# Kernel tuning notes

Measured on AMD Instinct MI355X. Metric: run time of the kernel, lower is better.

## Reference

```python
import jax, jax.numpy as jnp
import numpy as np

B, C_IN, C_OUT, N = 8, 256, 128, 4096
BN_EPS = 1e-5


def _conv1x1(w, b, t):
    # w: [out, in], t: [B, in, N] -> [B, out, N]
    return jnp.einsum('oc,bcn->bon', w, t) + b[None, :, None]


def setup_inputs() -> dict:
    key = jax.random.key(0)
    ks = jax.random.split(key, 11)
    s_in = 1.0 / np.sqrt(C_IN)
    s_out = 1.0 / np.sqrt(C_OUT)
    return {
        'x': jax.random.normal(ks[0], (B, C_IN, N), dtype=jnp.float32),
        'g_w': jax.random.normal(ks[1], (C_OUT, C_IN), dtype=jnp.float32) * s_in,
        'g_b': jax.random.normal(ks[2], (C_OUT,), dtype=jnp.float32) * s_in,
        'theta_w': jax.random.normal(ks[3], (C_OUT, C_IN), dtype=jnp.float32) * s_in,
        'theta_b': jax.random.normal(ks[4], (C_OUT,), dtype=jnp.float32) * s_in,
        'phi_w': jax.random.normal(ks[5], (C_OUT, C_IN), dtype=jnp.float32) * s_in,
        'phi_b': jax.random.normal(ks[6], (C_OUT,), dtype=jnp.float32) * s_in,
        'W_w': jax.random.normal(ks[7], (C_IN, C_OUT), dtype=jnp.float32) * s_out,
        'W_b': jax.random.normal(ks[8], (C_IN,), dtype=jnp.float32) * s_out,
        'bn_gamma': jax.random.uniform(ks[9], (C_IN,), dtype=jnp.float32),
        'bn_beta': jax.random.normal(ks[10], (C_IN,), dtype=jnp.float32) * 0.1,
    }


def reference(x, g_w, g_b, theta_w, theta_b, phi_w, phi_b, W_w, W_b, bn_gamma, bn_beta):
    n = x.shape[-1]
    g_x = _conv1x1(g_w, g_b, x)          # [B, Co, N]
    theta_x = _conv1x1(theta_w, theta_b, x)  # [B, Co, N]
    phi_x = _conv1x1(phi_w, phi_b, x)        # [B, Co, N]
    # f = theta_x^T @ phi_x, divided by N (no softmax) -> [B, N, N]
    f_div_c = jnp.einsum('bcn,bcm->bnm', theta_x, phi_x) / n
    # y[b,c,n] = sum_m f[b,n,m] * g_x[b,c,m]  -> already permuted to [B, Co, N]
    y = jnp.einsum('bnm,bcm->bcn', f_div_c, g_x)
    w_y = jnp.einsum('oc,bcn->bon', W_w, y) + W_b[None, :, None]  # [B, C_in, N]
    # BatchNorm1d, training mode: stats over (batch, spatial), biased variance
    mean = w_y.mean(axis=(0, 2), keepdims=True)
    var = w_y.var(axis=(0, 2), keepdims=True)
    w_y = (w_y - mean) * jax.lax.rsqrt(var + BN_EPS)
    w_y = w_y * bn_gamma[None, :, None] + bn_beta[None, :, None]
    return w_y + x  # generate=True residual
```

## Files before the change

kernel.cpp:

```cpp
#include <hip/hip_runtime.h>
#include <hip/hip_bf16.h>
#include <stdint.h>

#define BB   8
#define CIN  256
#define COUT 128
#define NN   4096

using f32x4  = __attribute__((ext_vector_type(4))) float;
using bf16x8 = __attribute__((ext_vector_type(8))) __bf16;
using u16x8  = __attribute__((ext_vector_type(8))) unsigned short;

static __device__ __forceinline__ unsigned short f2bf(float f) {
    unsigned int u = __builtin_bit_cast(unsigned int, f);
    u += 0x7FFFu + ((u >> 16) & 1u);
    return (unsigned short)(u >> 16);
}
static __device__ __forceinline__ float bf2f(unsigned short u) {
    return __builtin_bit_cast(float, (unsigned int)u << 16);
}
static __device__ __forceinline__ ushort4 pack4(float a, float b, float c, float d) {
    ushort4 r; r.x=f2bf(a); r.y=f2bf(b); r.z=f2bf(c); r.w=f2bf(d); return r;
}
#define MFMA(a,b,c) __builtin_amdgcn_mfma_f32_16x16x32_bf16((a),(b),(c),0,0,0)

static __device__ __forceinline__ int sw256(int r, int c) { return (r*256 + c) ^ ((r&7)<<3); }
static __device__ __forceinline__ int sw128(int r, int c) { return (r*128 + c) ^ ((r&7)<<3); }

__global__ __launch_bounds__(512) void kA(
    const float* __restrict__ x,
    const float* __restrict__ Wwf, const float* __restrict__ gwf,
    const float* __restrict__ twf, const float* __restrict__ pwf,
    const float* __restrict__ gbv, const float* __restrict__ pbv, const float* __restrict__ tbv,
    unsigned short* __restrict__ Sp, float* __restrict__ Rp,
    unsigned short* __restrict__ Abf, unsigned short* __restrict__ CmT,
    float* __restrict__ a1, float* __restrict__ c1v, float* __restrict__ p2,
    float* __restrict__ params, float* __restrict__ stats)
{
    __shared__ __align__(16) unsigned short SH[65536];
    int bid = blockIdx.x;
    int t = threadIdx.x, lane = t & 63, wv = t >> 6;
    int lr = lane & 15, lg = lane >> 4;

    if (bid < 128) {
        int b = bid >> 4, ch = bid & 15;
        int n0 = ch * 256;
        const float* xb = x + (size_t)b*CIN*NN + n0 + lane*4;
        #pragma unroll
        for (int g = 0; g < 2; ++g) {
            float4 v[16];
            #pragma unroll
            for (int i = 0; i < 16; ++i) {
                int c = wv*32 + g*16 + i;
                v[i] = *(const float4*)(xb + (size_t)c*NN);
            }
            #pragma unroll
            for (int i = 0; i < 16; ++i) {
                int c = wv*32 + g*16 + i;
                *(ushort4*)&SH[sw256(c, lane*4)] = pack4(v[i].x, v[i].y, v[i].z, v[i].w);
            }
        }
        __syncthreads();

        int wr = wv >> 1, wc = wv & 1;
        f32x4 acc[4][8];
        #pragma unroll
        for (int i = 0; i < 4; ++i)
            #pragma unroll
            for (int j = 0; j < 8; ++j) acc[i][j] = (f32x4){0.f,0.f,0.f,0.f};
        #pragma unroll
        for (int ks = 0; ks < 8; ++ks) {
            bf16x8 af[4], bfr[8];
            #pragma unroll
            for (int mi = 0; mi < 4; ++mi) {
                int row = wr*64 + mi*16 + lr;
                af[mi] = __builtin_bit_cast(bf16x8, *(const u16x8*)&SH[sw256(row, ks*32 + lg*8)]);
            }
            #pragma unroll
            for (int ni = 0; ni < 8; ++ni) {
                int row = wc*128 + ni*16 + lr;
                bfr[ni] = __builtin_bit_cast(bf16x8, *(const u16x8*)&SH[sw256(row, ks*32 + lg*8)]);
            }
            #pragma unroll
            for (int mi = 0; mi < 4; ++mi)
                #pragma unroll
                for (int ni = 0; ni < 8; ++ni)
                    acc[mi][ni] = MFMA(af[mi], bfr[ni], acc[mi][ni]);
        }
        if (t < 256) {
            float s = 0.f;
            #pragma unroll
            for (int q = 0; q < 32; ++q) {
                u16x8 vv = *(const u16x8*)&SH[sw256(t, q*8)];
                #pragma unroll
                for (int e = 0; e < 8; ++e) s += bf2f(vv[e]);
            }
            Rp[bid*256 + t] = s;
        }
        __syncthreads();
        #pragma unroll
        for (int mi = 0; mi < 4; ++mi)
            #pragma unroll
            for (int ni = 0; ni < 8; ++ni)
                #pragma unroll
                for (int j = 0; j < 4; ++j) {
                    int c1 = wr*64 + mi*16 + lg*4 + j;
                    int c2 = wc*128 + ni*16 + lr;
                    SH[sw256(c1, c2)] = f2bf(acc[mi][ni][j]);
                }
        __syncthreads();
        unsigned short* dst = Sp + (size_t)bid * 65536;
        #pragma unroll
        for (int i = t; i < 8192; i += 512) {
            int row = i >> 5, q = i & 31;
            *(u16x8*)(dst + row*256 + ((q ^ (row&7)) * 8)) = *(const u16x8*)&SH[row*256 + q*8];
        }
        return;
    }

    unsigned short* Ls = SH;
    unsigned short* Rs = SH + 32768;
    if (bid == 128) {
        for (int i = t; i < 8192; i += 512) {
            int flat = i*4, r = flat >> 7, c = flat & 127;
            float4 f = *(const float4*)(Wwf + flat);
            *(ushort4*)&Ls[sw128(r, c)] = pack4(f.x, f.y, f.z, f.w);
        }
        {
            int c = lane * 4;  int k4 = wv * 4;
            #pragma unroll
            for (int rep = 0; rep < 4; ++rep) {
                int kb = rep*32 + k4;
                float4 f0 = *(const float4*)(gwf + (size_t)(kb+0)*256 + c);
                float4 f1 = *(const float4*)(gwf + (size_t)(kb+1)*256 + c);
                float4 f2 = *(const float4*)(gwf + (size_t)(kb+2)*256 + c);
                float4 f3 = *(const float4*)(gwf + (size_t)(kb+3)*256 + c);
                *(ushort4*)&Rs[sw128(c+0, kb)] = pack4(f0.x, f1.x, f2.x, f3.x);
                *(ushort4*)&Rs[sw128(c+1, kb)] = pack4(f0.y, f1.y, f2.y, f3.y);
                *(ushort4*)&Rs[sw128(c+2, kb)] = pack4(f0.z, f1.z, f2.z, f3.z);
                *(ushort4*)&Rs[sw128(c+3, kb)] = pack4(f0.w, f1.w, f2.w, f3.w);
            }
        }
        if (t < 512) stats[t] = 0.f;
    } else {
        {
            int c = lane * 4;  int k4 = wv * 4;
            #pragma unroll
            for (int rep = 0; rep < 4; ++rep) {
                int kb = rep*32 + k4;
                float4 f0 = *(const float4*)(twf + (size_t)(kb+0)*256 + c);
                float4 f1 = *(const float4*)(twf + (size_t)(kb+1)*256 + c);
                float4 f2 = *(const float4*)(twf + (size_t)(kb+2)*256 + c);
                float4 f3 = *(const float4*)(twf + (size_t)(kb+3)*256 + c);
                *(ushort4*)&Ls[sw128(c+0, kb)] = pack4(f0.x, f1.x, f2.x, f3.x);
                *(ushort4*)&Ls[sw128(c+1, kb)] = pack4(f0.y, f1.y, f2.y, f3.y);
                *(ushort4*)&Ls[sw128(c+2, kb)] = pack4(f0.z, f1.z, f2.z, f3.z);
                *(ushort4*)&Ls[sw128(c+3, kb)] = pack4(f0.w, f1.w, f2.w, f3.w);
                float4 g0 = *(const float4*)(pwf + (size_t)(kb+0)*256 + c);
                float4 g1 = *(const float4*)(pwf + (size_t)(kb+1)*256 + c);
                float4 g2 = *(const float4*)(pwf + (size_t)(kb+2)*256 + c);
                float4 g3 = *(const float4*)(pwf + (size_t)(kb+3)*256 + c);
                *(ushort4*)&Rs[sw128(c+0, kb)] = pack4(g0.x, g1.x, g2.x, g3.x);
                *(ushort4*)&Rs[sw128(c+1, kb)] = pack4(g0.y, g1.y, g2.y, g3.y);
                *(ushort4*)&Rs[sw128(c+2, kb)] = pack4(g0.z, g1.z, g2.z, g3.z);
                *(ushort4*)&Rs[sw128(c+3, kb)] = pack4(g0.w, g1.w, g2.w, g3.w);
            }
        }
    }
    __syncthreads();

    int wr = wv >> 2, wc = wv & 3;
    f32x4 acc[8][4];
    #pragma unroll
    for (int i = 0; i < 8; ++i)
        #pragma unroll
        for (int j = 0; j < 4; ++j) acc[i][j] = (f32x4){0.f,0.f,0.f,0.f};
    #pragma unroll
    for (int ks = 0; ks < 4; ++ks) {
        bf16x8 af[8], bfr[4];
        #pragma unroll
        for (int mi = 0; mi < 8; ++mi) {
            int r = wr*128 + mi*16 + lr;
            af[mi] = __builtin_bit_cast(bf16x8, *(const u16x8*)&Ls[sw128(r, ks*32 + lg*8)]);
        }
        #pragma unroll
        for (int ni = 0; ni < 4; ++ni) {
            int c = wc*64 + ni*16 + lr;
            bfr[ni] = __builtin_bit_cast(bf16x8, *(const u16x8*)&Rs[sw128(c, ks*32 + lg*8)]);
        }
        #pragma unroll
        for (int mi = 0; mi < 8; ++mi)
            #pragma unroll
            for (int ni = 0; ni < 4; ++ni)
                acc[mi][ni] = MFMA(af[mi], bfr[ni], acc[mi][ni]);
    }
    unsigned short* Dst = (bid == 128) ? Abf : CmT;
    #pragma unroll
    for (int mi = 0; mi < 8; ++mi)
        #pragma unroll
        for (int ni = 0; ni < 4; ++ni)
            #pragma unroll
            for (int j = 0; j < 4; ++j) {
                int r = wr*128 + mi*16 + lg*4 + j;
                int c = wc*64 + ni*16 + lr;
                Dst[r*256 + c] = f2bf(acc[mi][ni][j]);
            }

    if (bid == 128) {
        if (t < 256) {
            float s = 0.f;
            #pragma unroll
            for (int q = 0; q < 32; ++q) {
                float4 f = *(const float4*)(Wwf + (size_t)t*128 + q*4);
                s += f.x*gbv[q*4] + f.y*gbv[q*4+1] + f.z*gbv[q*4+2] + f.w*gbv[q*4+3];
            }
            a1[t] = s;
        }
    } else {
        if (t < 256) {
            float s1 = 0.f, s2 = 0.f;
            for (int k = 0; k < 128; ++k) {
                s1 += twf[(size_t)k*256 + t] * pbv[k];
                s2 += pwf[(size_t)k*256 + t] * tbv[k];
            }
            c1v[t] = s1; p2[t] = s2;
        }
        if (t < 64) {
            float v = pbv[t]*tbv[t] + pbv[t+64]*tbv[t+64];
            #pragma unroll
            for (int off = 1; off < 64; off <<= 1) v += __shfl_xor(v, off);
            if (t == 0) params[0] = v;
        }
    }
}

__global__ __launch_bounds__(512) void kR(
    const unsigned short* __restrict__ Sp, const float* __restrict__ Rp,
    unsigned short* __restrict__ Sbf, float* __restrict__ rv)
{
    int bid = blockIdx.x, t = threadIdx.x;
    if (bid < 128) {
        int b = bid >> 4, sl = bid & 15;
        int base = sl*4096 + t*8;
        float s[8] = {0.f,0.f,0.f,0.f,0.f,0.f,0.f,0.f};
        #pragma unroll
        for (int i = 0; i < 16; ++i) {
            u16x8 v = *(const u16x8*)(Sp + (size_t)(b*16 + i)*65536 + base);
            #pragma unroll
            for (int e = 0; e < 8; ++e) s[e] += bf2f(v[e]);
        }
        u16x8 o;
        #pragma unroll
        for (int e = 0; e < 8; ++e) o[e] = f2bf(s[e]);
        *(u16x8*)(Sbf + (size_t)b*65536 + base) = o;
    } else {
        int b = bid - 128;
        if (t < 256) {
            float s = 0.f;
            #pragma unroll
            for (int i = 0; i < 16; ++i) s += Rp[(b*16 + i)*256 + t];
            rv[b*256 + t] = s;
        }
    }
}

__global__ __launch_bounds__(512) void kE(
    const unsigned short* __restrict__ Sbf, const float* __restrict__ rv,
    const unsigned short* __restrict__ Abf, const unsigned short* __restrict__ CmT,
    const float* __restrict__ a1g, const float* __restrict__ c1vg, const float* __restrict__ p2g,
    const float* __restrict__ params, const float* __restrict__ Wbv,
    unsigned short* __restrict__ Ebf, float* __restrict__ fv, float* __restrict__ stats)
{
    __shared__ __align__(16) unsigned short Ybuf[16384];
    __shared__ __align__(16) unsigned short Ebuf[16384];
    __shared__ float r_l[256], p2_l[256], c1v_l[256], cr[256];
    __shared__ float a1_l[64], ar[64], Yp2[64], er[64], diag_l[64];
    __shared__ float rp2_s;
    int blk = blockIdx.x;
    int b = blk >> 2, obase = (blk & 3) * 64;
    int t = threadIdx.x, lane = t & 63, wv = t >> 6;
    int lr = lane & 15, lg = lane >> 4;
    const float invN = 1.0f/4096.0f;
    const unsigned short* Sb = Sbf + (size_t)b*65536;

    if (t < 256) {
        r_l[t] = rv[b*256 + t];
        p2_l[t] = p2g[t];
        c1v_l[t] = c1vg[t];
    } else if (t < 320) {
        a1_l[t - 256] = a1g[obase + (t - 256)];
    }
    __syncthreads();

    f32x4 acc[4][2];
    #pragma unroll
    for (int i = 0; i < 4; ++i) { acc[i][0] = (f32x4){0,0,0,0}; acc[i][1] = (f32x4){0,0,0,0}; }
    const unsigned short* Arow0 = Abf + (size_t)obase*256;
    #pragma unroll
    for (int ks = 0; ks < 8; ++ks) {
        bf16x8 a4[4], b2[2];
        #pragma unroll
        for (int mi = 0; mi < 4; ++mi)
            a4[mi] = __builtin_bit_cast(bf16x8, *(const u16x8*)(Arow0 + (size_t)(mi*16+lr)*256 + ks*32 + lg*8));
        #pragma unroll
        for (int ni = 0; ni < 2; ++ni)
            b2[ni] = __builtin_bit_cast(bf16x8, *(const u16x8*)(Sb + (size_t)(wv*32+ni*16+lr)*256 + ks*32 + lg*8));
        #pragma unroll
        for (int mi = 0; mi < 4; ++mi)
            #pragma unroll
            for (int ni = 0; ni < 2; ++ni)
                acc[mi][ni] = MFMA(a4[mi], b2[ni], acc[mi][ni]);
    }
    #pragma unroll
    for (int mi = 0; mi < 4; ++mi)
        #pragma unroll
        for (int ni = 0; ni < 2; ++ni)
            #pragma unroll
            for (int j = 0; j < 4; ++j) {
                int ol = mi*16 + lg*4 + j;
                int c2 = wv*32 + ni*16 + lr;
                Ybuf[ol*256 + (c2 ^ ((ol&7)<<3))] = f2bf(acc[mi][ni][j]);
            }
    __syncthreads();

    {
        int row = t >> 3, p8 = t & 7;
        float sA = 0.f, sY = 0.f;
        const unsigned short* Ar = Abf + (size_t)(obase + row)*256 + p8*32;
        #pragma unroll
        for (int q = 0; q < 4; ++q) {
            u16x8 av = *(const u16x8*)(Ar + q*8);
            #pragma unroll
            for (int e = 0; e < 8; ++e) {
                int c = p8*32 + q*8 + e;
                sA += bf2f(av[e]) * r_l[c];
                sY += bf2f(Ybuf[row*256 + (c ^ ((row&7)<<3))]) * p2_l[c];
            }
        }
        sA += __shfl_xor(sA, 1); sA += __shfl_xor(sA, 2); sA += __shfl_xor(sA, 4);
        sY += __shfl_xor(sY, 1); sY += __shfl_xor(sY, 2); sY += __shfl_xor(sY, 4);
        if (p8 == 0) { ar[row] = sA; Yp2[row] = sY; }
    }
    if (t < 256) {
        float s = 0.f;
        const unsigned short* Cr = CmT + (size_t)t*256;
        #pragma unroll
        for (int q = 0; q < 32; ++q) {
            u16x8 v = *(const u16x8*)(Cr + q*8);
            #pragma unroll
            for (int e = 0; e < 8; ++e) s += bf2f(v[e]) * r_l[q*8 + e];
        }
        cr[t] = s;
    }
    if (t < 64) {
        float v = r_l[t*4]*p2_l[t*4] + r_l[t*4+1]*p2_l[t*4+1]
                + r_l[t*4+2]*p2_l[t*4+2] + r_l[t*4+3]*p2_l[t*4+3];
        #pragma unroll
        for (int off = 1; off < 64; off <<= 1) v += __shfl_xor(v, off);
        if (t == 0) rp2_s = v;
    }
    __syncthreads();

    f32x4 accE[4][2];
    #pragma unroll
    for (int i = 0; i < 4; ++i) { accE[i][0] = (f32x4){0,0,0,0}; accE[i][1] = (f32x4){0,0,0,0}; }
    #pragma unroll
    for (int ks = 0; ks < 8; ++ks) {
        bf16x8 a4[4], b2[2];
        #pragma unroll
        for (int mi = 0; mi < 4; ++mi) {
            int ol = mi*16 + lr;
            a4[mi] = __builtin_bit_cast(bf16x8, *(const u16x8*)&Ybuf[ol*256 + ((ks*32 + lg*8) ^ ((ol&7)<<3))]);
        }
        #pragma unroll
        for (int ni = 0; ni < 2; ++ni)
            b2[ni] = __builtin_bit_cast(bf16x8, *(const u16x8*)(CmT + (size_t)(wv*32+ni*16+lr)*256 + ks*32 + lg*8));
        #pragma unroll
        for (int mi = 0; mi < 4; ++mi)
            #pragma unroll
            for (int ni = 0; ni < 2; ++ni)
                accE[mi][ni] = MFMA(a4[mi], b2[ni], accE[mi][ni]);
    }
    unsigned short* Eb = Ebf + (size_t)b*65536;
    #pragma unroll
    for (int mi = 0; mi < 4; ++mi)
        #pragma unroll
        for (int ni = 0; ni < 2; ++ni)
            #pragma unroll
            for (int j = 0; j < 4; ++j) {
                int ol = mi*16 + lg*4 + j;
                int cp = wv*32 + ni*16 + lr;
                float e = accE[mi][ni][j]*invN + a1_l[ol]*invN*cr[cp]
                        + (invN*ar[ol] + a1_l[ol])*c1v_l[cp];
                unsigned short eb = f2bf(e);
                Ebuf[ol*256 + (cp ^ ((ol&7)<<3))] = eb;
                Eb[(size_t)(obase + ol)*256 + cp] = eb;
            }
    __syncthreads();

    float f_reg = 0.f;
    {
        int row = t >> 3, p8 = t & 7;
        float s = 0.f;
        #pragma unroll
        for (int q = 0; q < 4; ++q)
            #pragma unroll
            for (int e = 0; e < 8; ++e) {
                int c = p8*32 + q*8 + e;
                s += bf2f(Ebuf[row*256 + (c ^ ((row&7)<<3))]) * r_l[c];
            }
        s += __shfl_xor(s, 1); s += __shfl_xor(s, 2); s += __shfl_xor(s, 4);
        if (p8 == 0) er[row] = s;
    }
    if (t < 64) {
        diag_l[t] = 0.f;
        float sg = params[0];
        f_reg = invN*(Yp2[t] + a1_l[t]*rp2_s + ar[t]*sg) + a1_l[t]*sg + Wbv[obase + t];
        fv[b*256 + obase + t] = f_reg;
    }
    __syncthreads();

    f32x4 accZ[4][2];
    #pragma unroll
    for (int i = 0; i < 4; ++i) { accZ[i][0] = (f32x4){0,0,0,0}; accZ[i][1] = (f32x4){0,0,0,0}; }
    #pragma unroll
    for (int ks = 0; ks < 8; ++ks) {
        bf16x8 a4[4], b2[2];
        #pragma unroll
        for (int mi = 0; mi < 4; ++mi) {
            int ol = mi*16 + lr;
            a4[mi] = __builtin_bit_cast(bf16x8, *(const u16x8*)&Ebuf[ol*256 + ((ks*32 + lg*8) ^ ((ol&7)<<3))]);
        }
        #pragma unroll
        for (int ni = 0; ni < 2; ++ni)
            b2[ni] = __builtin_bit_cast(bf16x8, *(const u16x8*)(Sb + (size_t)(wv*32+ni*16+lr)*256 + ks*32 + lg*8));
        #pragma unroll
        for (int mi = 0; mi < 4; ++mi)
            #pragma unroll
            for (int ni = 0; ni < 2; ++ni)
                accZ[mi][ni] = MFMA(a4[mi], b2[ni], accZ[mi][ni]);
    }
    #pragma unroll
    for (int mi = 0; mi < 4; ++mi)
        #pragma unroll
        for (int j = 0; j < 4; ++j) {
            int ol = mi*16 + lg*4 + j;
            float s = 0.f;
            #pragma unroll
            for (int ni = 0; ni < 2; ++ni) {
                int c2 = wv*32 + ni*16 + lr;
                s += accZ[mi][ni][j] * bf2f(Ebuf[ol*256 + (c2 ^ ((ol&7)<<3))]);
            }
            s += __shfl_xor(s, 1); s += __shfl_xor(s, 2);
            s += __shfl_xor(s, 4); s += __shfl_xor(s, 8);
            if (lr == 0) atomicAdd(&diag_l[ol], s);
        }
    __syncthreads();

    if (t < 64) {
        int o = obase + t;
        atomicAdd(&stats[o], er[t] + 4096.0f*f_reg);
        atomicAdd(&stats[256 + o], diag_l[t] + 2.0f*f_reg*er[t] + 4096.0f*f_reg*f_reg);
    }
}

__global__ __launch_bounds__(512) void kF(
    const float* __restrict__ x, const unsigned short* __restrict__ Ebf,
    const float* __restrict__ fv, const float* __restrict__ stats,
    const float* __restrict__ gamma, const float* __restrict__ beta,
    float* __restrict__ out)
{
    __shared__ __align__(16) unsigned short Xs[128*256];
    __shared__ float scale_l[256], shift_l[256];
    int b = blockIdx.x >> 5, n0 = (blockIdx.x & 31) * 128;
    int t = threadIdx.x, lane = t & 63, wv = t >> 6, lr = lane & 15, lg = lane >> 4;
    const float inv = 1.0f / 32768.0f;
    if (t < 256) {
        float mu  = stats[t] * inv;
        float var = stats[256 + t] * inv - mu*mu;
        float sc  = gamma[t] * rsqrtf(var + 1e-5f);
        scale_l[t] = sc;
        shift_l[t] = (fv[b*256 + t] - mu) * sc + beta[t];
    }
    {
        int nq = (t & 31) * 4, c0 = (t >> 5) * 4;
        const float* xb = x + (size_t)b*CIN*NN + n0 + nq;
        #pragma unroll
        for (int p = 0; p < 4; ++p) {
            int c = p*64 + c0;
            const float* xp = xb + (size_t)c*NN;
            float4 f0 = *(const float4*)(xp);
            float4 f1 = *(const float4*)(xp + NN);
            float4 f2 = *(const float4*)(xp + 2*NN);
            float4 f3 = *(const float4*)(xp + 3*NN);
            *(ushort4*)&Xs[(nq+0)*256 + (c ^ (((nq+0)&7)<<3))] = pack4(f0.x,f1.x,f2.x,f3.x);
            *(ushort4*)&Xs[(nq+1)*256 + (c ^ (((nq+1)&7)<<3))] = pack4(f0.y,f1.y,f2.y,f3.y);
            *(ushort4*)&Xs[(nq+2)*256 + (c ^ (((nq+2)&7)<<3))] = pack4(f0.z,f1.z,f2.z,f3.z);
            *(ushort4*)&Xs[(nq+3)*256 + (c ^ (((nq+3)&7)<<3))] = pack4(f0.w,f1.w,f2.w,f3.w);
        }
    }
    __syncthreads();

    int wn = wv >> 2, wo = wv & 3;
    int nb = wn*64, ob = wo*64;
    const unsigned short* Eb = Ebf + (size_t)b*65536;
    f32x4 acc[4][4];
    #pragma unroll
    for (int i = 0; i < 4; ++i)
        #pragma unroll
        for (int j = 0; j < 4; ++j) acc[i][j] = (f32x4){0,0,0,0};

    #pragma unroll
    for (int ks = 0; ks < 8; ++ks) {
        bf16x8 xf[4], ef[4];
        #pragma unroll
        for (int ni = 0; ni < 4; ++ni) {
            int n = nb + ni*16 + lr;
            xf[ni] = __builtin_bit_cast(bf16x8, *(const u16x8*)&Xs[(n*256 + ks*32 + lg*8) ^ ((n&7)<<3)]);
        }
        #pragma unroll
        for (int oi = 0; oi < 4; ++oi) {
            int o = ob + oi*16 + lr;
            ef[oi] = __builtin_bit_cast(bf16x8, *(const u16x8*)(Eb + (size_t)o*256 + ks*32 + lg*8));
        }
        #pragma unroll
        for (int oi = 0; oi < 4; ++oi)
            #pragma unroll
            for (int ni = 0; ni < 4; ++ni)
                acc[oi][ni] = MFMA(ef[oi], xf[ni], acc[oi][ni]);
    }

    float* op = out + (size_t)b*CIN*NN + n0;
    #pragma unroll
    for (int oi = 0; oi < 4; ++oi) {
        #pragma unroll
        for (int j = 0; j < 4; ++j) {
            int o = ob + oi*16 + lg*4 + j;
            float sc = scale_l[o], sh = shift_l[o];
            #pragma unroll
            for (int ni = 0; ni < 4; ++ni) {
                int n = nb + ni*16 + lr;
                float val = acc[oi][ni][j]*sc + sh + bf2f(Xs[(n*256 + (o ^ ((n&7)<<3)))]);
                op[(size_t)o*NN + n] = val;
            }
        }
    }
}

extern "C" void kernel_launch(void* const* d_in, const int* in_sizes, int n_in,
                              void* d_out, int out_size, void* d_ws, size_t ws_size,
                              hipStream_t stream)
{
    (void)in_sizes; (void)n_in; (void)out_size; (void)ws_size;
    const float* x     = (const float*)d_in[0];
    const float* gw    = (const float*)d_in[1];
    const float* gb    = (const float*)d_in[2];
    const float* tw    = (const float*)d_in[3];
    const float* tb    = (const float*)d_in[4];
    const float* pw    = (const float*)d_in[5];
    const float* pb    = (const float*)d_in[6];
    const float* Ww    = (const float*)d_in[7];
    const float* Wb    = (const float*)d_in[8];
    const float* gamma = (const float*)d_in[9];
    const float* beta  = (const float*)d_in[10];
    float* out = (float*)d_out;

    char* ws = (char*)d_ws;
    unsigned short* Sp  = (unsigned short*)(ws + 0);
    float* Rp           = (float*)(ws + 16777216);
    unsigned short* Sbf = (unsigned short*)(ws + 16908288);
    float* rv           = (float*)(ws + 17956864);
    unsigned short* Abf = (unsigned short*)(ws + 17965056);
    unsigned short* CmT = (unsigned short*)(ws + 18096128);
    unsigned short* Ebf = (unsigned short*)(ws + 18227200);
    float* fv           = (float*)(ws + 19275776);
    float* a1           = (float*)(ws + 19283968);
    float* c1v          = (float*)(ws + 19284992);
    float* p2           = (float*)(ws + 19286016);
    float* params       = (float*)(ws + 19287040);
    float* stats        = (float*)(ws + 19287104);

    kA<<<130, 512, 0, stream>>>(x, Ww, gw, tw, pw, gb, pb, tb,
                                Sp, Rp, Abf, CmT, a1, c1v, p2, params, stats);
    kR<<<136, 512, 0, stream>>>(Sp, Rp, Sbf, rv);
    kE<<<32,  512, 0, stream>>>(Sbf, rv, Abf, CmT, a1, c1v, p2, params, Wb, Ebf, fv, stats);
    kF<<<256, 512, 0, stream>>>(x, Ebf, fv, stats, gamma, beta, out);
}
```

Measured before the change: 83.15 us.

## Split Gram kernel to 1024 threads and move weight-product blocks into reduction kernel

The x^T x Gram-tile kernel now runs with 1024 threads per block using a 4x4 wave grid with smaller per-wave accumulators. The two weight-product blocks (Ww·gw and theta/phi products) move out of it into the reduction kernel, where they run alongside the partial-sum reduction. The goal is to cut register pressure, raise MFMA parallelism in the first kernel, and take the slower weight-product blocks off its critical path. The final kernel's x loading is also reorganized to issue eight loads before packing, which raises memory-level parallelism.

```diff
diff --git a/kernel.cpp b/kernel.cpp
--- a/kernel.cpp
+++ b/kernel.cpp
@@ -27,100 +27,133 @@
 static __device__ __forceinline__ int sw256(int r, int c) { return (r*256 + c) ^ ((r&7)<<3); }
 static __device__ __forceinline__ int sw128(int r, int c) { return (r*128 + c) ^ ((r&7)<<3); }
 
-__global__ __launch_bounds__(512) void kA(
+__global__ __launch_bounds__(1024) void kA(
     const float* __restrict__ x,
+    unsigned short* __restrict__ Sp, float* __restrict__ Rp)
+{
+    __shared__ __align__(16) unsigned short SH[65536];
+    int bid = blockIdx.x;
+    int b = bid >> 4, ch = bid & 15;
+    int n0 = ch * 256;
+    int t = threadIdx.x, lane = t & 63, wv = t >> 6;
+    int lr = lane & 15, lg = lane >> 4;
+
+    const float* xb = x + (size_t)b*CIN*NN + n0 + lane*4;
+    #pragma unroll
+    for (int g = 0; g < 2; ++g) {
+        float4 v[8];
+        #pragma unroll
+        for (int i = 0; i < 8; ++i) {
+            int c = wv*16 + g*8 + i;
+            v[i] = *(const float4*)(xb + (size_t)c*NN);
+        }
+        #pragma unroll
+        for (int i = 0; i < 8; ++i) {
+            int c = wv*16 + g*8 + i;
+            *(ushort4*)&SH[sw256(c, lane*4)] = pack4(v[i].x, v[i].y, v[i].z, v[i].w);
+        }
+    }
+    __syncthreads();
+
+    int wr = wv >> 2, wc = wv & 3;
+    f32x4 acc[4][4];
+    #pragma unroll
+    for (int i = 0; i < 4; ++i)
+        #pragma unroll
+        for (int j = 0; j < 4; ++j) acc[i][j] = (f32x4){0.f,0.f,0.f,0.f};
+    #pragma unroll
+    for (int ks = 0; ks < 8; ++ks) {
+        bf16x8 af[4], bfr[4];
+        #pragma unroll
+        for (int mi = 0; mi < 4; ++mi) {
+            int row = wr*64 + mi*16 + lr;
+            af[mi] = __builtin_bit_cast(bf16x8, *(const u16x8*)&SH[sw256(row, ks*32 + lg*8)]);
+        }
+        #pragma unroll
+        for (int ni = 0; ni < 4; ++ni) {
+            int row = wc*64 + ni*16 + lr;
+            bfr[ni] = __builtin_bit_cast(bf16x8, *(const u16x8*)&SH[sw256(row, ks*32 + lg*8)]);
+        }
+        #pragma unroll
+        for (int mi = 0; mi < 4; ++mi)
+            #pragma unroll
+            for (int ni = 0; ni < 4; ++ni)
+                acc[mi][ni] = MFMA(af[mi], bfr[ni], acc[mi][ni]);
+    }
+    if (t < 256) {
+        float s = 0.f;
+        #pragma unroll
+        for (int q = 0; q < 32; ++q) {
+            u16x8 vv = *(const u16x8*)&SH[sw256(t, q*8)];
+            #pragma unroll
+            for (int e = 0; e < 8; ++e) s += bf2f(vv[e]);
+        }
+        Rp[bid*256 + t] = s;
+    }
+    __syncthreads();
+    #pragma unroll
+    for (int mi = 0; mi < 4; ++mi)
+        #pragma unroll
+        for (int ni = 0; ni < 4; ++ni)
+            #pragma unroll
+            for (int j = 0; j < 4; ++j) {
+                int c1 = wr*64 + mi*16 + lg*4 + j;
+                int c2 = wc*64 + ni*16 + lr;
+                SH[sw256(c1, c2)] = f2bf(acc[mi][ni][j]);
+            }
+    __syncthreads();
+    unsigned short* dst = Sp + (size_t)bid * 65536;
+    #pragma unroll
+    for (int i = t; i < 8192; i += 1024) {
+        int row = i >> 5, q = i & 31;
+        *(u16x8*)(dst + row*256 + ((q ^ (row&7)) * 8)) = *(const u16x8*)&SH[row*256 + q*8];
+    }
+}
+
+__global__ __launch_bounds__(512) void kR(
+    const unsigned short* __restrict__ Sp, const float* __restrict__ Rp,
     const float* __restrict__ Wwf, const float* __restrict__ gwf,
     const float* __restrict__ twf, const float* __restrict__ pwf,
     const float* __restrict__ gbv, const float* __restrict__ pbv, const float* __restrict__ tbv,
-    unsigned short* __restrict__ Sp, float* __restrict__ Rp,
+    unsigned short* __restrict__ Sbf, float* __restrict__ rv,
     unsigned short* __restrict__ Abf, unsigned short* __restrict__ CmT,
     float* __restrict__ a1, float* __restrict__ c1v, float* __restrict__ p2,
     float* __restrict__ params, float* __restrict__ stats)
 {
-    __shared__ __align__(16) unsigned short SH[65536];
+    __shared__ __align__(16) unsigned short Ls[32768];
+    __shared__ __align__(16) unsigned short Rs[32768];
     int bid = blockIdx.x;
     int t = threadIdx.x, lane = t & 63, wv = t >> 6;
     int lr = lane & 15, lg = lane >> 4;
 
     if (bid < 128) {
-        int b = bid >> 4, ch = bid & 15;
-        int n0 = ch * 256;
-        const float* xb = x + (size_t)b*CIN*NN + n0 + lane*4;
-        #pragma unroll
-        for (int g = 0; g < 2; ++g) {
-            float4 v[16];
-            #pragma unroll
-            for (int i = 0; i < 16; ++i) {
-                int c = wv*32 + g*16 + i;
-                v[i] = *(const float4*)(xb + (size_t)c*NN);
-            }
-            #pragma unroll
-            for (int i = 0; i < 16; ++i) {
-                int c = wv*32 + g*16 + i;
-                *(ushort4*)&SH[sw256(c, lane*4)] = pack4(v[i].x, v[i].y, v[i].z, v[i].w);
-            }
-        }
-        __syncthreads();
-
-        int wr = wv >> 1, wc = wv & 1;
-        f32x4 acc[4][8];
-        #pragma unroll
-        for (int i = 0; i < 4; ++i)
-            #pragma unroll
-            for (int j = 0; j < 8; ++j) acc[i][j] = (f32x4){0.f,0.f,0.f,0.f};
-        #pragma unroll
-        for (int ks = 0; ks < 8; ++ks) {
-            bf16x8 af[4], bfr[8];
-            #pragma unroll
-            for (int mi = 0; mi < 4; ++mi) {
-                int row = wr*64 + mi*16 + lr;
-                af[mi] = __builtin_bit_cast(bf16x8, *(const u16x8*)&SH[sw256(row, ks*32 + lg*8)]);
-            }
-            #pragma unroll
-            for (int ni = 0; ni < 8; ++ni) {
-                int row = wc*128 + ni*16 + lr;
-                bfr[ni] = __builtin_bit_cast(bf16x8, *(const u16x8*)&SH[sw256(row, ks*32 + lg*8)]);
-            }
-            #pragma unroll
-            for (int mi = 0; mi < 4; ++mi)
-                #pragma unroll
-                for (int ni = 0; ni < 8; ++ni)
-                    acc[mi][ni] = MFMA(af[mi], bfr[ni], acc[mi][ni]);
-        }
+        int b = bid >> 4, sl = bid & 15;
+        int base = sl*4096 + t*8;
+        float s[8] = {0.f,0.f,0.f,0.f,0.f,0.f,0.f,0.f};
+        #pragma unroll
+        for (int i = 0; i < 16; ++i) {
+            u16x8 v = *(const u16x8*)(Sp + (size_t)(b*16 + i)*65536 + base);
+            #pragma unroll
+            for (int e = 0; e < 8; ++e) s[e] += bf2f(v[e]);
+        }
+        u16x8 o;
+        #pragma unroll
+        for (int e = 0; e < 8; ++e) o[e] = f2bf(s[e]);
+        *(u16x8*)(Sbf + (size_t)b*65536 + base) = o;
+        return;
+    }
+    if (bid < 136) {
+        int b = bid - 128;
         if (t < 256) {
             float s = 0.f;
             #pragma unroll
-            for (int q = 0; q < 32; ++q) {
-                u16x8 vv = *(const u16x8*)&SH[sw256(t, q*8)];
-                #pragma unroll
-                for (int e = 0; e < 8; ++e) s += bf2f(vv[e]);
-            }
-            Rp[bid*256 + t] = s;
-        }
-        __syncthreads();
-        #pragma unroll
-        for (int mi = 0; mi < 4; ++mi)
-            #pragma unroll
-            for (int ni = 0; ni < 8; ++ni)
-                #pragma unroll
-                for (int j = 0; j < 4; ++j) {
-                    int c1 = wr*64 + mi*16 + lg*4 + j;
-                    int c2 = wc*128 + ni*16 + lr;
-                    SH[sw256(c1, c2)] = f2bf(acc[mi][ni][j]);
-                }
-        __syncthreads();
-        unsigned short* dst = Sp + (size_t)bid * 65536;
-        #pragma unroll
-        for (int i = t; i < 8192; i += 512) {
-            int row = i >> 5, q = i & 31;
-            *(u16x8*)(dst + row*256 + ((q ^ (row&7)) * 8)) = *(const u16x8*)&SH[row*256 + q*8];
+            for (int i = 0; i < 16; ++i) s += Rp[(b*16 + i)*256 + t];
+            rv[b*256 + t] = s;
         }
         return;
     }
 
-    unsigned short* Ls = SH;
-    unsigned short* Rs = SH + 32768;
-    if (bid == 128) {
+    if (bid == 136) {
         for (int i = t; i < 8192; i += 512) {
             int flat = i*4, r = flat >> 7, c = flat & 127;
             float4 f = *(const float4*)(Wwf + flat);
@@ -194,7 +227,7 @@
             for (int ni = 0; ni < 4; ++ni)
                 acc[mi][ni] = MFMA(af[mi], bfr[ni], acc[mi][ni]);
     }
-    unsigned short* Dst = (bid == 128) ? Abf : CmT;
+    unsigned short* Dst = (bid == 136) ? Abf : CmT;
     #pragma unroll
     for (int mi = 0; mi < 8; ++mi)
         #pragma unroll
@@ -206,7 +239,7 @@
                 Dst[r*256 + c] = f2bf(acc[mi][ni][j]);
             }
 
-    if (bid == 128) {
+    if (bid == 136) {
         if (t < 256) {
             float s = 0.f;
             #pragma unroll
@@ -230,36 +263,6 @@
             #pragma unroll
             for (int off = 1; off < 64; off <<= 1) v += __shfl_xor(v, off);
             if (t == 0) params[0] = v;
-        }
-    }
-}
-
-__global__ __launch_bounds__(512) void kR(
-    const unsigned short* __restrict__ Sp, const float* __restrict__ Rp,
-    unsigned short* __restrict__ Sbf, float* __restrict__ rv)
-{
-    int bid = blockIdx.x, t = threadIdx.x;
-    if (bid < 128) {
-        int b = bid >> 4, sl = bid & 15;
-        int base = sl*4096 + t*8;
-        float s[8] = {0.f,0.f,0.f,0.f,0.f,0.f,0.f,0.f};
-        #pragma unroll
-        for (int i = 0; i < 16; ++i) {
-            u16x8 v = *(const u16x8*)(Sp + (size_t)(b*16 + i)*65536 + base);
-            #pragma unroll
-            for (int e = 0; e < 8; ++e) s[e] += bf2f(v[e]);
-        }
-        u16x8 o;
-        #pragma unroll
-        for (int e = 0; e < 8; ++e) o[e] = f2bf(s[e]);
-        *(u16x8*)(Sbf + (size_t)b*65536 + base) = o;
-    } else {
-        int b = bid - 128;
-        if (t < 256) {
-            float s = 0.f;
-            #pragma unroll
-            for (int i = 0; i < 16; ++i) s += Rp[(b*16 + i)*256 + t];
-            rv[b*256 + t] = s;
         }
     }
 }
@@ -486,17 +489,25 @@
         int nq = (t & 31) * 4, c0 = (t >> 5) * 4;
         const float* xb = x + (size_t)b*CIN*NN + n0 + nq;
         #pragma unroll
-        for (int p = 0; p < 4; ++p) {
-            int c = p*64 + c0;
-            const float* xp = xb + (size_t)c*NN;
-            float4 f0 = *(const float4*)(xp);
-            float4 f1 = *(const float4*)(xp + NN);
-            float4 f2 = *(const float4*)(xp + 2*NN);
-            float4 f3 = *(const float4*)(xp + 3*NN);
-            *(ushort4*)&Xs[(nq+0)*256 + (c ^ (((nq+0)&7)<<3))] = pack4(f0.x,f1.x,f2.x,f3.x);
-            *(ushort4*)&Xs[(nq+1)*256 + (c ^ (((nq+1)&7)<<3))] = pack4(f0.y,f1.y,f2.y,f3.y);
-            *(ushort4*)&Xs[(nq+2)*256 + (c ^ (((nq+2)&7)<<3))] = pack4(f0.z,f1.z,f2.z,f3.z);
-            *(ushort4*)&Xs[(nq+3)*256 + (c ^ (((nq+3)&7)<<3))] = pack4(f0.w,f1.w,f2.w,f3.w);
+        for (int h = 0; h < 2; ++h) {
+            float4 f[8];
+            #pragma unroll
+            for (int p = 0; p < 2; ++p) {
+                int c = (h*2 + p)*64 + c0;
+                const float* xp = xb + (size_t)c*NN;
+                f[p*4+0] = *(const float4*)(xp);
+                f[p*4+1] = *(const float4*)(xp + NN);
+                f[p*4+2] = *(const float4*)(xp + 2*NN);
+                f[p*4+3] = *(const float4*)(xp + 3*NN);
+            }
+            #pragma unroll
+            for (int p = 0; p < 2; ++p) {
+                int c = (h*2 + p)*64 + c0;
+                *(ushort4*)&Xs[(nq+0)*256 + (c ^ (((nq+0)&7)<<3))] = pack4(f[p*4].x, f[p*4+1].x, f[p*4+2].x, f[p*4+3].x);
+                *(ushort4*)&Xs[(nq+1)*256 + (c ^ (((nq+1)&7)<<3))] = pack4(f[p*4].y, f[p*4+1].y, f[p*4+2].y, f[p*4+3].y);
+                *(ushort4*)&Xs[(nq+2)*256 + (c ^ (((nq+2)&7)<<3))] = pack4(f[p*4].z, f[p*4+1].z, f[p*4+2].z, f[p*4+3].z);
+                *(ushort4*)&Xs[(nq+3)*256 + (c ^ (((nq+3)&7)<<3))] = pack4(f[p*4].w, f[p*4+1].w, f[p*4+2].w, f[p*4+3].w);
+            }
         }
     }
     __syncthreads();
@@ -580,9 +591,9 @@
     float* params       = (float*)(ws + 19287040);
     float* stats        = (float*)(ws + 19287104);
 
-    kA<<<130, 512, 0, stream>>>(x, Ww, gw, tw, pw, gb, pb, tb,
-                                Sp, Rp, Abf, CmT, a1, c1v, p2, params, stats);
-    kR<<<136, 512, 0, stream>>>(Sp, Rp, Sbf, rv);
-    kE<<<32,  512, 0, stream>>>(Sbf, rv, Abf, CmT, a1, c1v, p2, params, Wb, Ebf, fv, stats);
-    kF<<<256, 512, 0, stream>>>(x, Ebf, fv, stats, gamma, beta, out);
-}
+    kA<<<128, 1024, 0, stream>>>(x, Sp, Rp);
+    kR<<<138, 512,  0, stream>>>(Sp, Rp, Ww, gw, tw, pw, gb, pb, tb,
+                                 Sbf, rv, Abf, CmT, a1, c1v, p2, params, stats);
+    kE<<<32,  512,  0, stream>>>(Sbf, rv, Abf, CmT, a1, c1v, p2, params, Wb, Ebf, fv, stats);
+    kF<<<256, 512,  0, stream>>>(x, Ebf, fv, stats, gamma, beta, out);
+}
```

After: 91.38 us. +9.9%, slower.
